# Kernel tuning notes

Measured on AMD Instinct MI355X. Metric: run time of the kernel, lower is better.

The kernel has to match this reference:

```python
import jax, jax.numpy as jnp
import numpy as np
import math

EPS = 1e-5  # torch BatchNorm2d default eps
EXPANSION_RATE = 2


def _bn_train(x, gamma, beta):
    # BatchNorm2d in training mode: biased batch statistics over (B, H, W)
    mu = jnp.mean(x, axis=(0, 2, 3), keepdims=True)
    var = jnp.var(x, axis=(0, 2, 3), keepdims=True)
    xn = (x - mu) * jax.lax.rsqrt(var + EPS)
    return gamma[None, :, None, None] * xn + beta[None, :, None, None]


def _conv1x1(x, w, b):
    # w: [O, C]  (1x1 conv kernel squeezed), b: [O]
    return jnp.einsum('bchw,oc->bohw', x, w) + b[None, :, None, None]


def _lsgc(x, w_diff, b_diff, g_bn, be_bn, w_in, b_in, g_ibn, be_ibn,
          w_mr, b_mr, g_mbn, be_mbn):
    B, C, H, W = x.shape
    bit_depth = max(math.ceil(math.log2(H)), math.ceil(math.log2(W)))
    steps = [EXPANSION_RATE * 2 ** (n - 1) for n in range(1, bit_depth + 1)]

    fmax = None
    for step in steps:
        for axis, size in ((3, W), (2, H)):
            s = step % size
            for sgn in (1, -1):  # forward / backward rolls
                shifted = jnp.roll(x, sgn * s, axis=axis) if s else x
                d = x - shifted
                fmax = d if fmax is None else jnp.maximum(fmax, d)

    x_diff = _bn_train(_conv1x1(fmax, w_diff, b_diff), g_bn, be_bn)
    x_proc = _bn_train(_conv1x1(x, w_in, b_in), g_ibn, be_ibn)

    # MRConv: concat -> 1x1 conv -> BN -> GELU (exact) -> residual add
    x_cat = jnp.concatenate([x_proc, x_diff], axis=1)
    h = _bn_train(_conv1x1(x_cat, w_mr, b_mr), g_mbn, be_mbn)
    h = jax.nn.gelu(h, approximate=False)
    return x_proc + h


def setup_inputs() -> dict:
    key = jax.random.key(0)
    ks = jax.random.split(key, 8)
    B, C_in, C_out, H, W = 32, 128, 128, 64, 64

    def kaiming(k, o, i):
        return jax.random.normal(k, (o, i), jnp.float32) * np.sqrt(2.0 / i)

    return {
        'x': jax.random.normal(ks[0], (B, C_in, H, W), jnp.float32),
        'w_diff': kaiming(ks[1], C_out, C_in),
        'b_diff': jnp.zeros((C_out,), jnp.float32),
        'g_bn': jnp.ones((C_out,), jnp.float32),
        'be_bn': jnp.zeros((C_out,), jnp.float32),
        'w_in': kaiming(ks[2], C_out, C_in),
        'b_in': jnp.zeros((C_out,), jnp.float32),
        'g_ibn': jnp.ones((C_out,), jnp.float32),
        'be_ibn': jnp.zeros((C_out,), jnp.float32),
        'w_mr': kaiming(ks[3], C_out, 2 * C_out),
        'b_mr': jnp.zeros((C_out,), jnp.float32),
        'g_mbn': jnp.ones((C_out,), jnp.float32),
        'be_mbn': jnp.zeros((C_out,), jnp.float32),
    }


def reference(x, w_diff, b_diff, g_bn, be_bn, w_in, b_in, g_ibn, be_ibn,
              w_mr, b_mr, g_mbn, be_mbn):
    return _lsgc(x, w_diff, b_diff, g_bn, be_bn, w_in, b_in, g_ibn, be_ibn,
                 w_mr, b_mr, g_mbn, be_mbn)
```

## Files before the change

### kernel.cpp

```cpp
#include <hip/hip_runtime.h>
#include <math.h>


#define INV_NPIX (1.0f / 131072.0f)
#define EPS 1e-5f
#define KP 66

typedef __attribute__((ext_vector_type(8))) short s16x8;
typedef __attribute__((ext_vector_type(4))) float f32x4;

__device__ __forceinline__ uint32_t bf16_rne(float v) {
  uint32_t x = __float_as_uint(v);
  return (x + 0x7fffu + ((x >> 16) & 1u)) >> 16;
}
__device__ __forceinline__ uint32_t pack_hl(float v) {
  uint32_t h = bf16_rne(v);
  float lo = v - __uint_as_float(h << 16);
  return h | (bf16_rne(lo) << 16);
}
__device__ __forceinline__ float bf_lo(uint32_t d) {
  return __uint_as_float(d << 16);
}
__device__ __forceinline__ float bf_hi(uint32_t d) {
  return __uint_as_float(d & 0xffff0000u);
}
__device__ __forceinline__ float4 fmin4(float4 a, float4 b) {
  return make_float4(fminf(a.x, b.x), fminf(a.y, b.y), fminf(a.z, b.z),
                     fminf(a.w, b.w));
}

__global__ __launch_bounds__(256) void stencil_prep_kernel(
    const float* __restrict__ x, uint32_t* __restrict__ xp,
    uint32_t* __restrict__ fp, const float* __restrict__ w_in,
    const float* __restrict__ w_diff, unsigned short* __restrict__ wInH,
    unsigned short* __restrict__ wInL, unsigned short* __restrict__ wDfH,
    unsigned short* __restrict__ wDfL, float* __restrict__ stats) {
  __shared__ float4 pA[1024];
  __shared__ float4 pB[1024];
  if (blockIdx.x >= 2048) {
    const int t = (blockIdx.x - 2048) * 256 + threadIdx.x;
    if (t < 24576) stats[t] = 0.f;
    const int e = t & 16383;
    const float* w = (t < 16384) ? w_in : w_diff;
    unsigned short* aH = (t < 16384) ? wInH : wDfH;
    unsigned short* aL = (t < 16384) ? wInL : wDfL;
    const int j = e & 7, l = (e >> 3) & 63, mt = (e >> 9) & 7, kc = e >> 12;
    const int m = mt * 16 + (l & 15);
    const int k = kc * 32 + ((l >> 4) << 3) + j;
    const uint32_t p = pack_hl(w[m * 128 + k]);
    aH[e] = (unsigned short)(p & 0xffffu);
    aL[e] = (unsigned short)(p >> 16);
    return;
  }
  const int b = blockIdx.x >> 6;
  const int cp = blockIdx.x & 63;
  const float4* xa = (const float4*)x + (size_t)(b * 128 + 2 * cp) * 1024;
  const float4* xb = xa + 1024;
  float4 sA[4], sB[4];
#pragma unroll
  for (int i = 0; i < 4; ++i) {
    const int u = threadIdx.x + i * 256;
    sA[i] = xa[u];
    sB[i] = xb[u];
    pA[u] = sA[i];
    pB[u] = sB[i];
  }
  __syncthreads();
  const size_t obase = (size_t)(b * 64 + cp) * 1024;
#pragma unroll
  for (int i = 0; i < 4; ++i) {
    const int u = threadIdx.x + i * 256;
    const int h = u >> 4, wu = u & 15;
    const int row = u & ~15;
    float4 mA, mB;
    {
      const float4 A = sA[i];
      const float4 L = pA[row | ((wu + 15) & 15)];
      const float4 R = pA[row | ((wu + 1) & 15)];
      float4 m = fmin4(A, fmin4(L, R));
      m = fmin4(m, make_float4(A.z, A.w, R.x, R.y));
      m = fmin4(m, make_float4(L.z, L.w, A.x, A.y));
      m = fmin4(m, pA[row | ((wu + 2) & 15)]);
      m = fmin4(m, pA[row | ((wu + 14) & 15)]);
      m = fmin4(m, pA[row | ((wu + 4) & 15)]);
      m = fmin4(m, pA[row | ((wu + 12) & 15)]);
      m = fmin4(m, pA[row | ((wu + 8) & 15)]);
      m = fmin4(m, pA[(((h + 2) & 63) << 4) | wu]);
      m = fmin4(m, pA[(((h + 62) & 63) << 4) | wu]);
      m = fmin4(m, pA[(((h + 4) & 63) << 4) | wu]);
      m = fmin4(m, pA[(((h + 60) & 63) << 4) | wu]);
      m = fmin4(m, pA[(((h + 8) & 63) << 4) | wu]);
      m = fmin4(m, pA[(((h + 56) & 63) << 4) | wu]);
      m = fmin4(m, pA[(((h + 16) & 63) << 4) | wu]);
      m = fmin4(m, pA[(((h + 48) & 63) << 4) | wu]);
      m = fmin4(m, pA[(((h + 32) & 63) << 4) | wu]);
      mA = m;
    }
    {
      const float4 A = sB[i];
      const float4 L = pB[row | ((wu + 15) & 15)];
      const float4 R = pB[row | ((wu + 1) & 15)];
      float4 m = fmin4(A, fmin4(L, R));
      m = fmin4(m, make_float4(A.z, A.w, R.x, R.y));
      m = fmin4(m, make_float4(L.z, L.w, A.x, A.y));
      m = fmin4(m, pB[row | ((wu + 2) & 15)]);
      m = fmin4(m, pB[row | ((wu + 14) & 15)]);
      m = fmin4(m, pB[row | ((wu + 4) & 15)]);
      m = fmin4(m, pB[row | ((wu + 12) & 15)]);
      m = fmin4(m, pB[row | ((wu + 8) & 15)]);
      m = fmin4(m, pB[(((h + 2) & 63) << 4) | wu]);
      m = fmin4(m, pB[(((h + 62) & 63) << 4) | wu]);
      m = fmin4(m, pB[(((h + 4) & 63) << 4) | wu]);
      m = fmin4(m, pB[(((h + 60) & 63) << 4) | wu]);
      m = fmin4(m, pB[(((h + 8) & 63) << 4) | wu]);
      m = fmin4(m, pB[(((h + 56) & 63) << 4) | wu]);
      m = fmin4(m, pB[(((h + 16) & 63) << 4) | wu]);
      m = fmin4(m, pB[(((h + 48) & 63) << 4) | wu]);
      m = fmin4(m, pB[(((h + 32) & 63) << 4) | wu]);
      mB = m;
    }
    uint4 px, pf;
    px.x = bf16_rne(sA[i].x) | (bf16_rne(sB[i].x) << 16);
    px.y = bf16_rne(sA[i].y) | (bf16_rne(sB[i].y) << 16);
    px.z = bf16_rne(sA[i].z) | (bf16_rne(sB[i].z) << 16);
    px.w = bf16_rne(sA[i].w) | (bf16_rne(sB[i].w) << 16);
    pf.x = bf16_rne(sA[i].x - mA.x) | (bf16_rne(sB[i].x - mB.x) << 16);
    pf.y = bf16_rne(sA[i].y - mA.y) | (bf16_rne(sB[i].y - mB.y) << 16);
    pf.z = bf16_rne(sA[i].z - mA.z) | (bf16_rne(sB[i].z - mB.z) << 16);
    pf.w = bf16_rne(sA[i].w - mA.w) | (bf16_rne(sB[i].w - mB.w) << 16);
    ((uint4*)xp)[obase + u] = px;
    ((uint4*)fp)[obase + u] = pf;
  }
}

template <int NC>
__device__ __forceinline__ void gemm_body(
    const unsigned short* __restrict__ AH, const unsigned short* __restrict__ AL,
    const uint32_t* __restrict__ B0, const uint32_t* __restrict__ B1,
    uint32_t* __restrict__ outp, float* __restrict__ sumv,
    float* __restrict__ sumq, const int bx, uint32_t* Bs) {
  const int tid = threadIdx.x;
  const int lane = tid & 63;
  const int wave = tid >> 6;
  const int b = bx >> 6;
  const int hw0 = (bx & 63) << 6;
  const int sk2 = tid >> 4;
  const int sn4 = (tid & 15) << 2;
  const int q = lane >> 4;
  const int ln = lane & 15;

  f32x4 acc[2][4];
#pragma unroll
  for (int i = 0; i < 2; ++i)
#pragma unroll
    for (int j = 0; j < 4; ++j) acc[i][j] = (f32x4)(0.0f);

  uint4 ld[4];
#pragma unroll
  for (int c = 0; c < 4; ++c)
    ld[c] = *(const uint4*)&B0[((size_t)(b * 64 + c * 16 + sk2)) * 4096 + hw0 +
                               sn4];

#pragma unroll
  for (int kc = 0; kc < NC; ++kc) {
    const int slot = kc & 3;
    uint32_t* buf = Bs + (kc & 1) * (16 * KP);
    *(uint4*)&buf[sk2 * KP + sn4] = ld[slot];
    s16x8 ah[2], al[2];
#pragma unroll
    for (int mt2 = 0; mt2 < 2; ++mt2) {
      const size_t off = ((size_t)((kc * 8 + wave * 2 + mt2) * 64 + lane)) << 3;
      ah[mt2] = *(const s16x8*)(AH + off);
      al[mt2] = *(const s16x8*)(AL + off);
    }
    if (NC == 8 && kc < 4) {
      ld[slot] = *(const uint4*)&B1[((size_t)(b * 64 + kc * 16 + sk2)) * 4096 +
                                    hw0 + sn4];
    }
    __syncthreads();
#pragma unroll
    for (int nt = 0; nt < 4; ++nt) {
      union { uint32_t u[4]; s16x8 s; } bb;
#pragma unroll
      for (int j = 0; j < 4; ++j)
        bb.u[j] = buf[(q * 4 + j) * KP + nt * 16 + ln];
#pragma unroll
      for (int mt2 = 0; mt2 < 2; ++mt2) {
        acc[mt2][nt] = __builtin_amdgcn_mfma_f32_16x16x32_bf16(
            ah[mt2], bb.s, acc[mt2][nt], 0, 0, 0);
        acc[mt2][nt] = __builtin_amdgcn_mfma_f32_16x16x32_bf16(
            al[mt2], bb.s, acc[mt2][nt], 0, 0, 0);
      }
    }
  }

  const int cb = (bx & 31) * 128;
#pragma unroll
  for (int mt2 = 0; mt2 < 2; ++mt2) {
    float sa[4] = {0.f, 0.f, 0.f, 0.f};
    float sq[4] = {0.f, 0.f, 0.f, 0.f};
#pragma unroll
    for (int nt = 0; nt < 4; ++nt) {
#pragma unroll
      for (int rp = 0; rp < 2; ++rp) {
        const float v0 = acc[mt2][nt][2 * rp];
        const float v1 = acc[mt2][nt][2 * rp + 1];
        const int m2 = (wave * 2 + mt2) * 8 + q * 2 + rp;
        outp[((size_t)(b * 64 + m2)) * 4096 + hw0 + nt * 16 + ln] =
            bf16_rne(v0) | (bf16_rne(v1) << 16);
        sa[2 * rp] += v0;
        sq[2 * rp] += v0 * v0;
        sa[2 * rp + 1] += v1;
        sq[2 * rp + 1] += v1 * v1;
      }
    }
#pragma unroll
    for (int off = 1; off < 16; off <<= 1) {
#pragma unroll
      for (int r = 0; r < 4; ++r) {
        sa[r] += __shfl_xor(sa[r], off);
        sq[r] += __shfl_xor(sq[r], off);
      }
    }
    if (ln == 0) {
#pragma unroll
      for (int r = 0; r < 4; ++r) {
        const int m = (wave * 2 + mt2) * 16 + q * 4 + r;
        atomicAdd(&sumv[cb + m], sa[r]);
        atomicAdd(&sumq[cb + m], sq[r]);
      }
    }
  }
}

__global__ __launch_bounds__(256) void gemm1_dual(
    const unsigned short* __restrict__ AH1, const unsigned short* __restrict__ AL1,
    const uint32_t* __restrict__ XP, uint32_t* __restrict__ out1,
    float* __restrict__ sv1, float* __restrict__ sq1,
    const unsigned short* __restrict__ AH2, const unsigned short* __restrict__ AL2,
    const uint32_t* __restrict__ FP, uint32_t* __restrict__ out2,
    float* __restrict__ sv2, float* __restrict__ sq2) {
  __shared__ uint32_t Bs[2 * 16 * KP];
  const int bx = blockIdx.x & 2047;
  if ((blockIdx.x >> 11) == 0)
    gemm_body<4>(AH1, AL1, XP, nullptr, out1, sv1, sq1, bx, Bs);
  else
    gemm_body<4>(AH2, AL2, FP, nullptr, out2, sv2, sq2, bx, Bs);
}

__global__ __launch_bounds__(256) void gemm2_kernel(
    const unsigned short* __restrict__ AH, const unsigned short* __restrict__ AL,
    const uint32_t* __restrict__ B0, const uint32_t* __restrict__ B1,
    uint32_t* __restrict__ outp, float* __restrict__ sv,
    float* __restrict__ sq) {
  __shared__ uint32_t Bs[2 * 16 * KP];
  gemm_body<8>(AH, AL, B0, B1, outp, sv, sq, blockIdx.x, Bs);
}

__global__ __launch_bounds__(256) void finalize1_kernel(
    const float* __restrict__ pSin, const float* __restrict__ pQin,
    const float* __restrict__ pSdf, const float* __restrict__ pQdf,
    const float* __restrict__ g_ibn, const float* __restrict__ be_ibn,
    const float* __restrict__ g_bn, const float* __restrict__ w_mr,
    float* __restrict__ a_in, float* __restrict__ d_in,
    unsigned short* __restrict__ wEffH, unsigned short* __restrict__ wEffL) {
  __shared__ float sa[256];
  const int t = threadIdx.x;
  if (t < 128) {
    float s = 0.f, qq = 0.f;
#pragma unroll
    for (int i = 0; i < 32; ++i) {
      s += pSin[i * 128 + t];
      qq += pQin[i * 128 + t];
    }
    const float mu = s * INV_NPIX;
    const float var = fmaxf(qq * INV_NPIX - mu * mu, 0.f);
    const float a = g_ibn[t] * rsqrtf(var + EPS);
    if (blockIdx.x == 0) {
      a_in[t] = a;
      d_in[t] = be_ibn[t] - mu * a;
    }
    sa[t] = a;
  } else {
    const int c = t - 128;
    float s = 0.f, qq = 0.f;
#pragma unroll
    for (int i = 0; i < 32; ++i) {
      s += pSdf[i * 128 + c];
      qq += pQdf[i * 128 + c];
    }
    const float mu = s * INV_NPIX;
    const float var = fmaxf(qq * INV_NPIX - mu * mu, 0.f);
    sa[t] = g_bn[c] * rsqrtf(var + EPS);
  }
  __syncthreads();
  const int e = blockIdx.x * 256 + t;
  const int j = e & 7, l = (e >> 3) & 63, mt = (e >> 9) & 7, kc = e >> 12;
  const int m = mt * 16 + (l & 15);
  const int k = kc * 32 + ((l >> 4) << 3) + j;
  const uint32_t p = pack_hl(w_mr[m * 256 + k] * sa[k]);
  wEffH[e] = (unsigned short)(p & 0xffffu);
  wEffL[e] = (unsigned short)(p >> 16);
}

__global__ __launch_bounds__(128) void finalize2_kernel(
    const float* __restrict__ pSh, const float* __restrict__ pQh,
    const float* __restrict__ g_mbn, const float* __restrict__ be_mbn,
    float* __restrict__ a_m, float* __restrict__ d_m) {
  const int t = threadIdx.x;
  float s = 0.f, qq = 0.f;
#pragma unroll
  for (int i = 0; i < 32; ++i) {
    s += pSh[i * 128 + t];
    qq += pQh[i * 128 + t];
  }
  const float mu = s * INV_NPIX;
  const float var = fmaxf(qq * INV_NPIX - mu * mu, 0.f);
  const float a = g_mbn[t] * rsqrtf(var + EPS);
  a_m[t] = a;
  d_m[t] = be_mbn[t] - mu * a;
}

__device__ __forceinline__ float gelu_exact(float z) {
  return 0.5f * z * (1.0f + erff(z * 0.70710678118654752f));
}

__global__ __launch_bounds__(256) void epilogue_kernel(
    const uint32_t* __restrict__ yp, const uint32_t* __restrict__ hp,
    const float* __restrict__ a_in, const float* __restrict__ d_in,
    const float* __restrict__ a_m, const float* __restrict__ d_m,
    float* __restrict__ out) {
  const size_t i = (size_t)blockIdx.x * 256 + threadIdx.x;
  const int cp = (int)((i >> 10) & 63);
  const int b = (int)(i >> 16);
  const int c0 = 2 * cp, c1 = 2 * cp + 1;
  const uint4 yv = ((const uint4*)yp)[i];
  const uint4 hv = ((const uint4*)hp)[i];
  const float a0 = a_in[c0], d0 = d_in[c0], m0 = a_m[c0], e0 = d_m[c0];
  const float a1 = a_in[c1], d1 = d_in[c1], m1 = a_m[c1], e1 = d_m[c1];
  float4 o0, o1;
  o0.x = fmaf(a0, bf_lo(yv.x), d0) + gelu_exact(fmaf(m0, bf_lo(hv.x), e0));
  o0.y = fmaf(a0, bf_lo(yv.y), d0) + gelu_exact(fmaf(m0, bf_lo(hv.y), e0));
  o0.z = fmaf(a0, bf_lo(yv.z), d0) + gelu_exact(fmaf(m0, bf_lo(hv.z), e0));
  o0.w = fmaf(a0, bf_lo(yv.w), d0) + gelu_exact(fmaf(m0, bf_lo(hv.w), e0));
  o1.x = fmaf(a1, bf_hi(yv.x), d1) + gelu_exact(fmaf(m1, bf_hi(hv.x), e1));
  o1.y = fmaf(a1, bf_hi(yv.y), d1) + gelu_exact(fmaf(m1, bf_hi(hv.y), e1));
  o1.z = fmaf(a1, bf_hi(yv.z), d1) + gelu_exact(fmaf(m1, bf_hi(hv.z), e1));
  o1.w = fmaf(a1, bf_hi(yv.w), d1) + gelu_exact(fmaf(m1, bf_hi(hv.w), e1));
  const size_t u = i & 1023;
  ((float4*)out)[(size_t)(b * 128 + c0) * 1024 + u] = o0;
  ((float4*)out)[(size_t)(b * 128 + c1) * 1024 + u] = o1;
}

extern "C" void kernel_launch(void* const* d_in, const int* in_sizes, int n_in,
                              void* d_out, int out_size, void* d_ws,
                              size_t ws_size, hipStream_t stream) {
  const float* x = (const float*)d_in[0];
  const float* w_diff = (const float*)d_in[1];
  const float* g_bn = (const float*)d_in[3];
  const float* w_in = (const float*)d_in[5];
  const float* g_ibn = (const float*)d_in[7];
  const float* be_ibn = (const float*)d_in[8];
  const float* w_mr = (const float*)d_in[9];
  const float* g_mbn = (const float*)d_in[11];
  const float* be_mbn = (const float*)d_in[12];
  float* out = (float*)d_out;

  const size_t PD = (size_t)8388608;
  uint32_t* ws = (uint32_t*)d_ws;
  uint32_t* xp = ws;
  uint32_t* fpx = ws + PD;
  uint32_t* ypIn = ws + 2 * PD;
  uint32_t* ypDf = ws + 3 * PD;
  uint32_t* hp = ws + 4 * PD;
  float* st = (float*)(ws + 5 * PD);
  float* pSin = st, *pQin = st + 4096;
  float* pSdf = st + 8192, *pQdf = st + 12288;
  float* pSh = st + 16384, *pQh = st + 20480;
  float* a_in = st + 24576, *dinc = st + 24704;
  float* a_m = st + 24832, *d_m = st + 24960;
  unsigned short* fr = (unsigned short*)(st + 25088);
  unsigned short* wInH = fr;
  unsigned short* wInL = fr + 16384;
  unsigned short* wDfH = fr + 32768;
  unsigned short* wDfL = fr + 49152;
  unsigned short* wEffH = fr + 65536;
  unsigned short* wEffL = fr + 98304;

  stencil_prep_kernel<<<2176, 256, 0, stream>>>(x, xp, fpx, w_in, w_diff,
                                                wInH, wInL, wDfH, wDfL, st);
  gemm1_dual<<<4096, 256, 0, stream>>>(wInH, wInL, xp, ypIn, pSin, pQin, wDfH,
                                       wDfL, fpx, ypDf, pSdf, pQdf);
  finalize1_kernel<<<128, 256, 0, stream>>>(pSin, pQin, pSdf, pQdf, g_ibn,
                                            be_ibn, g_bn, w_mr, a_in, dinc,
                                            wEffH, wEffL);
  gemm2_kernel<<<2048, 256, 0, stream>>>(wEffH, wEffL, ypIn, ypDf, hp, pSh,
                                         pQh);
  finalize2_kernel<<<1, 128, 0, stream>>>(pSh, pQh, g_mbn, be_mbn, a_m, d_m);
  epilogue_kernel<<<8192, 256, 0, stream>>>(ypIn, hp, a_in, dinc, a_m, d_m,
                                            out);
}
```

Measured before the change: 269.7 us.

## Replace BN-stat atomics with per-block partials plus reduction; prefetch A fragments

GEMM blocks now write per-block channel sums and sums of squares to scratch buffers instead of issuing float atomicAdds to 32 shared slots. Two new reduce kernels fold those partials before the finalize kernels, and the up-front zeroing of the stats buffer is dropped. Separately, the GEMM body loads all B tiles up front and double-buffers the A weight fragments one k-chunk ahead. The aim is to remove atomic contention and hide weight-load latency, at the cost of two extra launches, higher register pressure, and reuse of dead workspace regions for the partials.

```diff
diff --git a/kernel.cpp b/kernel.cpp
--- a/kernel.cpp
+++ b/kernel.cpp
@@ -34,12 +34,11 @@
     uint32_t* __restrict__ fp, const float* __restrict__ w_in,
     const float* __restrict__ w_diff, unsigned short* __restrict__ wInH,
     unsigned short* __restrict__ wInL, unsigned short* __restrict__ wDfH,
-    unsigned short* __restrict__ wDfL, float* __restrict__ stats) {
+    unsigned short* __restrict__ wDfL) {
   __shared__ float4 pA[1024];
   __shared__ float4 pB[1024];
   if (blockIdx.x >= 2048) {
     const int t = (blockIdx.x - 2048) * 256 + threadIdx.x;
-    if (t < 24576) stats[t] = 0.f;
     const int e = t & 16383;
     const float* w = (t < 16384) ? w_in : w_diff;
     unsigned short* aH = (t < 16384) ? wInH : wDfH;
@@ -137,8 +136,8 @@
 __device__ __forceinline__ void gemm_body(
     const unsigned short* __restrict__ AH, const unsigned short* __restrict__ AL,
     const uint32_t* __restrict__ B0, const uint32_t* __restrict__ B1,
-    uint32_t* __restrict__ outp, float* __restrict__ sumv,
-    float* __restrict__ sumq, const int bx, uint32_t* Bs) {
+    uint32_t* __restrict__ outp, float* __restrict__ pS,
+    float* __restrict__ pQ, const int bx, uint32_t* Bs) {
   const int tid = threadIdx.x;
   const int lane = tid & 63;
   const int wave = tid >> 6;
@@ -155,29 +154,37 @@
 #pragma unroll
     for (int j = 0; j < 4; ++j) acc[i][j] = (f32x4)(0.0f);
 
-  uint4 ld[4];
-#pragma unroll
-  for (int c = 0; c < 4; ++c)
-    ld[c] = *(const uint4*)&B0[((size_t)(b * 64 + c * 16 + sk2)) * 4096 + hw0 +
-                               sn4];
+  uint4 ld[NC];
+#pragma unroll
+  for (int c = 0; c < NC; ++c) {
+    const uint32_t* src = (c < 4) ? B0 : B1;
+    ld[c] = *(const uint4*)&src[((size_t)(b * 64 + (c & 3) * 16 + sk2)) * 4096 +
+                                hw0 + sn4];
+  }
+  s16x8 ah[2][2], al[2][2];
+#pragma unroll
+  for (int mt2 = 0; mt2 < 2; ++mt2) {
+    const size_t off = ((size_t)((wave * 2 + mt2) * 64 + lane)) << 3;
+    ah[0][mt2] = *(const s16x8*)(AH + off);
+    al[0][mt2] = *(const s16x8*)(AL + off);
+  }
 
 #pragma unroll
   for (int kc = 0; kc < NC; ++kc) {
-    const int slot = kc & 3;
-    uint32_t* buf = Bs + (kc & 1) * (16 * KP);
-    *(uint4*)&buf[sk2 * KP + sn4] = ld[slot];
-    s16x8 ah[2], al[2];
-#pragma unroll
-    for (int mt2 = 0; mt2 < 2; ++mt2) {
-      const size_t off = ((size_t)((kc * 8 + wave * 2 + mt2) * 64 + lane)) << 3;
-      ah[mt2] = *(const s16x8*)(AH + off);
-      al[mt2] = *(const s16x8*)(AL + off);
-    }
-    if (NC == 8 && kc < 4) {
-      ld[slot] = *(const uint4*)&B1[((size_t)(b * 64 + kc * 16 + sk2)) * 4096 +
-                                    hw0 + sn4];
-    }
+    const int cur = kc & 1;
+    const int nxt = cur ^ 1;
+    uint32_t* buf = Bs + cur * (16 * KP);
+    *(uint4*)&buf[sk2 * KP + sn4] = ld[kc];
     __syncthreads();
+    if (kc + 1 < NC) {
+#pragma unroll
+      for (int mt2 = 0; mt2 < 2; ++mt2) {
+        const size_t off =
+            ((size_t)(((kc + 1) * 8 + wave * 2 + mt2) * 64 + lane)) << 3;
+        ah[nxt][mt2] = *(const s16x8*)(AH + off);
+        al[nxt][mt2] = *(const s16x8*)(AL + off);
+      }
+    }
 #pragma unroll
     for (int nt = 0; nt < 4; ++nt) {
       union { uint32_t u[4]; s16x8 s; } bb;
@@ -187,14 +194,13 @@
 #pragma unroll
       for (int mt2 = 0; mt2 < 2; ++mt2) {
         acc[mt2][nt] = __builtin_amdgcn_mfma_f32_16x16x32_bf16(
-            ah[mt2], bb.s, acc[mt2][nt], 0, 0, 0);
+            ah[cur][mt2], bb.s, acc[mt2][nt], 0, 0, 0);
         acc[mt2][nt] = __builtin_amdgcn_mfma_f32_16x16x32_bf16(
-            al[mt2], bb.s, acc[mt2][nt], 0, 0, 0);
+            al[cur][mt2], bb.s, acc[mt2][nt], 0, 0, 0);
       }
     }
   }
 
-  const int cb = (bx & 31) * 128;
 #pragma unroll
   for (int mt2 = 0; mt2 < 2; ++mt2) {
     float sa[4] = {0.f, 0.f, 0.f, 0.f};
@@ -226,8 +232,8 @@
 #pragma unroll
       for (int r = 0; r < 4; ++r) {
         const int m = (wave * 2 + mt2) * 16 + q * 4 + r;
-        atomicAdd(&sumv[cb + m], sa[r]);
-        atomicAdd(&sumq[cb + m], sq[r]);
+        pS[bx * 128 + m] = sa[r];
+        pQ[bx * 128 + m] = sq[r];
       }
     }
   }
@@ -257,21 +263,39 @@
   gemm_body<8>(AH, AL, B0, B1, outp, sv, sq, blockIdx.x, Bs);
 }
 
+__global__ __launch_bounds__(256) void reduce_kernel(
+    const float* __restrict__ P, float* __restrict__ p2) {
+  const int a = blockIdx.x >> 4, g = blockIdx.x & 15;
+  const int c = threadIdx.x & 127, h = threadIdx.x >> 7;
+  const float* src = P + ((size_t)(a * 2048 + g * 128 + h * 64)) * 128 + c;
+  float s0 = 0.f, s1 = 0.f, s2 = 0.f, s3 = 0.f;
+#pragma unroll
+  for (int j = 0; j < 64; j += 4) {
+    s0 += src[(j + 0) * 128];
+    s1 += src[(j + 1) * 128];
+    s2 += src[(j + 2) * 128];
+    s3 += src[(j + 3) * 128];
+  }
+  __shared__ float sm[256];
+  sm[threadIdx.x] = (s0 + s1) + (s2 + s3);
+  __syncthreads();
+  if (h == 0) p2[(a * 16 + g) * 128 + c] = sm[c] + sm[128 + c];
+}
+
 __global__ __launch_bounds__(256) void finalize1_kernel(
-    const float* __restrict__ pSin, const float* __restrict__ pQin,
-    const float* __restrict__ pSdf, const float* __restrict__ pQdf,
-    const float* __restrict__ g_ibn, const float* __restrict__ be_ibn,
-    const float* __restrict__ g_bn, const float* __restrict__ w_mr,
-    float* __restrict__ a_in, float* __restrict__ d_in,
-    unsigned short* __restrict__ wEffH, unsigned short* __restrict__ wEffL) {
+    const float* __restrict__ p2, const float* __restrict__ g_ibn,
+    const float* __restrict__ be_ibn, const float* __restrict__ g_bn,
+    const float* __restrict__ w_mr, float* __restrict__ a_in,
+    float* __restrict__ d_in, unsigned short* __restrict__ wEffH,
+    unsigned short* __restrict__ wEffL) {
   __shared__ float sa[256];
   const int t = threadIdx.x;
   if (t < 128) {
     float s = 0.f, qq = 0.f;
 #pragma unroll
-    for (int i = 0; i < 32; ++i) {
-      s += pSin[i * 128 + t];
-      qq += pQin[i * 128 + t];
+    for (int g = 0; g < 16; ++g) {
+      s += p2[g * 128 + t];
+      qq += p2[(16 + g) * 128 + t];
     }
     const float mu = s * INV_NPIX;
     const float var = fmaxf(qq * INV_NPIX - mu * mu, 0.f);
@@ -285,9 +309,9 @@
     const int c = t - 128;
     float s = 0.f, qq = 0.f;
 #pragma unroll
-    for (int i = 0; i < 32; ++i) {
-      s += pSdf[i * 128 + c];
-      qq += pQdf[i * 128 + c];
+    for (int g = 0; g < 16; ++g) {
+      s += p2[(32 + g) * 128 + c];
+      qq += p2[(48 + g) * 128 + c];
     }
     const float mu = s * INV_NPIX;
     const float var = fmaxf(qq * INV_NPIX - mu * mu, 0.f);
@@ -304,15 +328,15 @@
 }
 
 __global__ __launch_bounds__(128) void finalize2_kernel(
-    const float* __restrict__ pSh, const float* __restrict__ pQh,
-    const float* __restrict__ g_mbn, const float* __restrict__ be_mbn,
-    float* __restrict__ a_m, float* __restrict__ d_m) {
+    const float* __restrict__ p2h, const float* __restrict__ g_mbn,
+    const float* __restrict__ be_mbn, float* __restrict__ a_m,
+    float* __restrict__ d_m) {
   const int t = threadIdx.x;
   float s = 0.f, qq = 0.f;
 #pragma unroll
-  for (int i = 0; i < 32; ++i) {
-    s += pSh[i * 128 + t];
-    qq += pQh[i * 128 + t];
+  for (int g = 0; g < 16; ++g) {
+    s += p2h[g * 128 + t];
+    qq += p2h[(16 + g) * 128 + t];
   }
   const float mu = s * INV_NPIX;
   const float var = fmaxf(qq * INV_NPIX - mu * mu, 0.f);
@@ -374,29 +398,32 @@
   uint32_t* ypDf = ws + 3 * PD;
   uint32_t* hp = ws + 4 * PD;
   float* st = (float*)(ws + 5 * PD);
-  float* pSin = st, *pQin = st + 4096;
-  float* pSdf = st + 8192, *pQdf = st + 12288;
-  float* pSh = st + 16384, *pQh = st + 20480;
-  float* a_in = st + 24576, *dinc = st + 24704;
-  float* a_m = st + 24832, *d_m = st + 24960;
-  unsigned short* fr = (unsigned short*)(st + 25088);
+  float* p2 = st;
+  float* p2h = st + 8192;
+  float* a_in = st + 12288, *dinc = st + 12416;
+  float* a_m = st + 12544, *d_m = st + 12672;
+  unsigned short* fr = (unsigned short*)(st + 12800);
   unsigned short* wInH = fr;
   unsigned short* wInL = fr + 16384;
   unsigned short* wDfH = fr + 32768;
   unsigned short* wDfL = fr + 49152;
   unsigned short* wEffH = fr + 65536;
   unsigned short* wEffL = fr + 98304;
+  float* g1p = (float*)(ws + 4 * PD);
+  float* g2p = (float*)ws;
 
   stencil_prep_kernel<<<2176, 256, 0, stream>>>(x, xp, fpx, w_in, w_diff,
-                                                wInH, wInL, wDfH, wDfL, st);
-  gemm1_dual<<<4096, 256, 0, stream>>>(wInH, wInL, xp, ypIn, pSin, pQin, wDfH,
-                                       wDfL, fpx, ypDf, pSdf, pQdf);
-  finalize1_kernel<<<128, 256, 0, stream>>>(pSin, pQin, pSdf, pQdf, g_ibn,
-                                            be_ibn, g_bn, w_mr, a_in, dinc,
-                                            wEffH, wEffL);
-  gemm2_kernel<<<2048, 256, 0, stream>>>(wEffH, wEffL, ypIn, ypDf, hp, pSh,
-                                         pQh);
-  finalize2_kernel<<<1, 128, 0, stream>>>(pSh, pQh, g_mbn, be_mbn, a_m, d_m);
+                                                wInH, wInL, wDfH, wDfL);
+  gemm1_dual<<<4096, 256, 0, stream>>>(wInH, wInL, xp, ypIn, g1p,
+                                       g1p + 262144, wDfH, wDfL, fpx, ypDf,
+                                       g1p + 524288, g1p + 786432);
+  reduce_kernel<<<64, 256, 0, stream>>>(g1p, p2);
+  finalize1_kernel<<<128, 256, 0, stream>>>(p2, g_ibn, be_ibn, g_bn, w_mr,
+                                            a_in, dinc, wEffH, wEffL);
+  gemm2_kernel<<<2048, 256, 0, stream>>>(wEffH, wEffL, ypIn, ypDf, hp, g2p,
+                                         g2p + 262144);
+  reduce_kernel<<<32, 256, 0, stream>>>(g2p, p2h);
+  finalize2_kernel<<<1, 128, 0, stream>>>(p2h, g_mbn, be_mbn, a_m, d_m);
   epilogue_kernel<<<8192, 256, 0, stream>>>(ypIn, hp, a_in, dinc, a_m, d_m,
                                             out);
 }
```

Measured after the change: 271.8 us. Within noise of the previous version (+0.8%).
